# Optimization experiments

Measured on AMD Instinct MI355X. Metric: run time of the kernel, lower is better.

## Reference

```python
import jax, jax.numpy as jnp
import numpy as np

DILATIONS = [1, 2, 4, 8, 12, 24]
NUM_ITER = 10
W1 = 0.3
EPS = 1e-8
# 8-neighborhood offsets of the one-hot 3x3 kernel (center excluded)
OFFSETS = [(0, 0), (0, 1), (0, 2), (1, 0), (1, 2), (2, 0), (2, 1), (2, 2)]


def resize_bilinear_ac(x, oh, ow):
    """Bilinear resize with align_corners=True on the last two dims."""
    H, W = x.shape[-2], x.shape[-1]
    ys = jnp.linspace(0.0, H - 1.0, oh)
    xs = jnp.linspace(0.0, W - 1.0, ow)
    y0 = jnp.floor(ys).astype(jnp.int32)
    y1 = jnp.minimum(y0 + 1, H - 1)
    wy = (ys - y0).astype(x.dtype)
    x0 = jnp.floor(xs).astype(jnp.int32)
    x1 = jnp.minimum(x0 + 1, W - 1)
    wx = (xs - x0).astype(x.dtype)
    r = x[..., y0, :] * (1.0 - wy)[:, None] + x[..., y1, :] * wy[:, None]
    return r[..., x0] * (1.0 - wx) + r[..., x1] * wx


def dilated_neighbors(x, dilations):
    """Replicate-pad + gather 8 dilated neighbors per dilation.
    x: [b,c,h,w] -> [b,c,8*len(dilations),h,w] (matches one-hot conv2d emulation)."""
    b, c, h, w = x.shape
    outs = []
    for d in dilations:
        xp = jnp.pad(x, ((0, 0), (0, 0), (d, d), (d, d)), mode='edge')
        for ki, kj in OFFSETS:
            outs.append(xp[:, :, d * ki:d * ki + h, d * kj:d * kj + w])
    return jnp.stack(outs, axis=2)


def make_pos(dilations):
    base = jnp.ones(8, dtype=jnp.float32)
    base = base.at[jnp.array([0, 2, 5, 7])].set(np.sqrt(2.0).astype(np.float32))
    return jnp.concatenate([base * d for d in dilations])  # [8*D]


def setup_inputs() -> dict:
    key = jax.random.key(0)
    k1, k2 = jax.random.split(key)
    imgs = jax.random.normal(k1, (1, 3, 224, 224), dtype=jnp.float32)
    masks = jax.random.uniform(k2, (1, 21, 56, 56), dtype=jnp.float32)
    return {"imgs": imgs, "masks": masks}


def reference(imgs, masks):
    b, c, h, w = imgs.shape
    # upsample masks to image resolution
    masks = resize_bilinear_ac(masks, h, w)
    # low-res branch (scale_factor=0.3, floor like torch)
    h2, w2 = int(h * 0.3), int(w * 0.3)
    imgs2 = resize_bilinear_ac(imgs, h2, w2)

    n2 = dilated_neighbors(imgs2, DILATIONS)                     # [1,3,K,h2,w2]
    abs2 = jnp.abs(n2 - imgs2[:, :, None])
    std2 = jnp.std(n2, axis=2, keepdims=True, ddof=1)
    aff2 = (-(abs2 / (std2 + EPS)) ** 2).mean(axis=1, keepdims=True)  # [1,1,K,h2,w2]

    n1 = dilated_neighbors(imgs, DILATIONS)                      # [1,3,K,h,w]
    abs1 = jnp.abs(n1 - imgs[:, :, None])
    std1 = jnp.std(n1, axis=2, keepdims=True, ddof=1)
    aff = (-(abs1 / (std1 + EPS) / W1) ** 2).mean(axis=1, keepdims=True)  # [1,1,K,h,w]

    pos = make_pos(DILATIONS)                                    # [K]
    pos_std = jnp.std(pos, ddof=1)
    pos_aff = -((pos / (pos_std + EPS) / W1) ** 2)               # [K]

    # squeeze(0) -> bilinear upsample -> unsqueeze(0)
    aff2_up = resize_bilinear_ac(aff2[0], h, w)[None]            # [1,1,K,h,w]

    aff_total = (jax.nn.softmax(aff, axis=2)
                 + jax.nn.softmax(aff2_up, axis=2)
                 + jax.nn.softmax(pos_aff)[None, None, :, None, None])

    for _ in range(NUM_ITER):
        nm = dilated_neighbors(masks, DILATIONS)                 # [1,21,K,h,w]
        masks = (nm * aff_total).sum(axis=2)
    return masks
```

## Files before the change

kernel.cpp:

```cpp
#include <hip/hip_runtime.h>
#include <hip/hip_fp16.h>
#include <math.h>

namespace {
constexpr int IH = 224, IW = 224;
constexpr int H2 = 67, W2 = 67;
constexpr int MH = 56, MW = 56;
constexpr int CI = 3, CM = 21;
constexpr int ND = 6;
constexpr int K = 48;
constexpr int HW = IH * IW;
constexpr int HW2 = H2 * W2;
constexpr float EPS = 1e-8f;
__device__ __constant__ int DILS_C[ND] = {1, 2, 4, 8, 12, 24};
}

struct PosArr { float v[K]; };

__device__ __forceinline__ float wsum64(float v) {
    #pragma unroll
    for (int off = 1; off < 64; off <<= 1) v += __shfl_xor(v, off);
    return v;
}

__device__ __forceinline__ void gload_lds16(const void* g, void* l) {
    __builtin_amdgcn_global_load_lds(
        (const __attribute__((address_space(1))) void*)(g),
        (__attribute__((address_space(3))) void*)(l), 16, 0, 0);
}

__global__ void k_prep(const float* __restrict__ img, float* __restrict__ img2,
                       const float* __restrict__ m, __half* __restrict__ mu) {
    int t = blockIdx.x * blockDim.x + threadIdx.x;
    if (t < CI * HW2) {
        int c = t / HW2, r = t % HW2;
        int y = r / W2, x = r % W2;
        float fy = (float)y * ((float)(IH - 1) / (float)(H2 - 1));
        float fx = (float)x * ((float)(IW - 1) / (float)(W2 - 1));
        int y0 = (int)floorf(fy); int y1 = min(y0 + 1, IH - 1); float wy = fy - (float)y0;
        int x0 = (int)floorf(fx); int x1 = min(x0 + 1, IW - 1); float wx = fx - (float)x0;
        const float* p = img + c * HW;
        float v00 = p[y0 * IW + x0], v01 = p[y0 * IW + x1];
        float v10 = p[y1 * IW + x0], v11 = p[y1 * IW + x1];
        float r0 = v00 * (1.f - wy) + v10 * wy;
        float r1 = v01 * (1.f - wy) + v11 * wy;
        img2[t] = r0 * (1.f - wx) + r1 * wx;
    }
    if (t < CM * HW) {
        int c = t / HW, r = t % HW;
        int y = r / IW, x = r % IW;
        float fy = (float)y * ((float)(MH - 1) / (float)(IH - 1));
        float fx = (float)x * ((float)(MW - 1) / (float)(IW - 1));
        int y0 = (int)floorf(fy); int y1 = min(y0 + 1, MH - 1); float wy = fy - (float)y0;
        int x0 = (int)floorf(fx); int x1 = min(x0 + 1, MW - 1); float wx = fx - (float)x0;
        const float* p = m + c * MH * MW;
        float v00 = p[y0 * MW + x0], v01 = p[y0 * MW + x1];
        float v10 = p[y1 * MW + x0], v11 = p[y1 * MW + x1];
        float r0 = v00 * (1.f - wy) + v10 * wy;
        float r1 = v01 * (1.f - wy) + v11 * wy;
        mu[t] = __float2half(r0 * (1.f - wx) + r1 * wx);
    }
}

__global__ void k_aff2(const float* __restrict__ img2, float* __restrict__ aff2) {
    int gtid = blockIdx.x * blockDim.x + threadIdx.x;
    int wave = gtid >> 6;
    int lane = threadIdx.x & 63;
    if (wave >= HW2) return;
    int t = wave;
    int y = t / W2, x = t % W2;

    int k = (lane < K) ? lane : (K - 1);
    int di = k >> 3, o = k & 7;
    int d = DILS_C[di];
    int ym = max(y - d, 0), yp = min(y + d, H2 - 1);
    int xm = max(x - d, 0), xp = min(x + d, W2 - 1);
    int ki = (0x22211000u >> (o * 4)) & 3;
    int kj = (0x21020210u >> (o * 4)) & 3;
    int ry = ki == 0 ? ym : (ki == 1 ? y : yp);
    int rx = kj == 0 ? xm : (kj == 1 ? x : xp);
    int nidx = ry * W2 + rx;

    float av = 0.f;
    #pragma unroll
    for (int c = 0; c < CI; ++c) {
        const float* p = img2 + c * HW2;
        float center = p[y * W2 + x];
        float v = p[nidx];
        float vv = (lane < K) ? v : 0.f;
        float s = wsum64(vv);
        float s2 = wsum64(vv * vv);
        float mean = s * (1.f / (float)K);
        float ss = s2 - (float)K * mean * mean;
        float stdv = sqrtf(fmaxf(ss, 0.f) * (1.f / (float)(K - 1)));
        float inv = 1.f / (stdv + EPS);
        float tt = fabsf(v - center) * inv;
        av += tt * tt;
    }
    if (lane < K) aff2[(size_t)t * K + k] = av;
}

__global__ void k_aff_total(const float* __restrict__ img,
                            const float* __restrict__ aff2,
                            __half* __restrict__ afft, PosArr pos) {
    int gid = blockIdx.x * blockDim.x + threadIdx.x;
    int t = gid >> 4;
    int lane = threadIdx.x & 15;
    if (t >= HW) return;
    int y = t / IW, x = t % IW;

    int nidx[3];
    int kk[3];
    #pragma unroll
    for (int s = 0; s < 3; ++s) {
        int k = lane + 16 * s;
        kk[s] = k;
        int di = k >> 3, o = k & 7;
        int d = DILS_C[di];
        int ki = (0x22211000u >> (o * 4)) & 3;
        int kj = (0x21020210u >> (o * 4)) & 3;
        int ym = max(y - d, 0), yp = min(y + d, IH - 1);
        int xm = max(x - d, 0), xp = min(x + d, IW - 1);
        int ry = ki == 0 ? ym : (ki == 1 ? y : yp);
        int rx = kj == 0 ? xm : (kj == 1 ? x : xp);
        nidx[s] = ry * IW + rx;
    }

    float av0 = 0.f, av1 = 0.f, av2 = 0.f;
    #pragma unroll
    for (int c = 0; c < CI; ++c) {
        const float* p = img + c * HW;
        float center = p[y * IW + x];
        float n0 = p[nidx[0]], n1 = p[nidx[1]], n2 = p[nidx[2]];
        float s1 = n0 + n1 + n2;
        float s2 = n0 * n0 + n1 * n1 + n2 * n2;
        #pragma unroll
        for (int off = 1; off < 16; off <<= 1) {
            s1 += __shfl_xor(s1, off, 16);
            s2 += __shfl_xor(s2, off, 16);
        }
        float mean = s1 * (1.f / (float)K);
        float ss = s2 - (float)K * mean * mean;
        float inv = 1.f / (sqrtf(fmaxf(ss, 0.f) * (1.f / (float)(K - 1))) + EPS);
        float t0 = fabsf(n0 - center) * inv; av0 += t0 * t0;
        float t1 = fabsf(n1 - center) * inv; av1 += t1 * t1;
        float t2 = fabsf(n2 - center) * inv; av2 += t2 * t2;
    }
    const float sc = -(1.f / (float)CI) / (0.3f * 0.3f);
    av0 *= sc; av1 *= sc; av2 *= sc;
    float m1 = fmaxf(av0, fmaxf(av1, av2));
    #pragma unroll
    for (int off = 1; off < 16; off <<= 1) m1 = fmaxf(m1, __shfl_xor(m1, off, 16));
    float e0 = expf(av0 - m1), e1 = expf(av1 - m1), e2 = expf(av2 - m1);
    float es = e0 + e1 + e2;
    #pragma unroll
    for (int off = 1; off < 16; off <<= 1) es += __shfl_xor(es, off, 16);
    float r1 = 1.f / es;

    float fy = (float)y * ((float)(H2 - 1) / (float)(IH - 1));
    float fx = (float)x * ((float)(W2 - 1) / (float)(IW - 1));
    int y0 = (int)floorf(fy); int y1 = min(y0 + 1, H2 - 1); float wy = fy - (float)y0;
    int x0 = (int)floorf(fx); int x1 = min(x0 + 1, W2 - 1); float wx = fx - (float)x0;
    const float* q00 = aff2 + (size_t)(y0 * W2 + x0) * K;
    const float* q01 = aff2 + (size_t)(y0 * W2 + x1) * K;
    const float* q10 = aff2 + (size_t)(y1 * W2 + x0) * K;
    const float* q11 = aff2 + (size_t)(y1 * W2 + x1) * K;
    float w00 = (1.f - wy) * (1.f - wx), w01 = (1.f - wy) * wx;
    float w10 = wy * (1.f - wx), w11 = wy * wx;
    const float sc2 = -(1.f / (float)CI);
    float b0 = (q00[kk[0]] * w00 + q01[kk[0]] * w01 + q10[kk[0]] * w10 + q11[kk[0]] * w11) * sc2;
    float b1 = (q00[kk[1]] * w00 + q01[kk[1]] * w01 + q10[kk[1]] * w10 + q11[kk[1]] * w11) * sc2;
    float b2 = (q00[kk[2]] * w00 + q01[kk[2]] * w01 + q10[kk[2]] * w10 + q11[kk[2]] * w11) * sc2;
    float m2 = fmaxf(b0, fmaxf(b1, b2));
    #pragma unroll
    for (int off = 1; off < 16; off <<= 1) m2 = fmaxf(m2, __shfl_xor(m2, off, 16));
    float f0 = expf(b0 - m2), f1 = expf(b1 - m2), f2 = expf(b2 - m2);
    float fs = f0 + f1 + f2;
    #pragma unroll
    for (int off = 1; off < 16; off <<= 1) fs += __shfl_xor(fs, off, 16);
    float r2 = 1.f / fs;

    __half* o = afft + (size_t)t * K;
    o[kk[0]] = __float2half(e0 * r1 + f0 * r2 + pos.v[kk[0]]);
    o[kk[1]] = __float2half(e1 * r1 + f1 * r2 + pos.v[kk[1]]);
    o[kk[2]] = __float2half(e2 * r1 + f2 * r2 + pos.v[kk[2]]);
}

template<bool LAST>
__global__ __launch_bounds__(256) void k_prop(const __half* __restrict__ min_,
                                              const __half* __restrict__ afft,
                                              void* __restrict__ mout) {
    __shared__ __half L[13 * 224];
    int tid = threadIdx.x;
    int bid = blockIdx.x;
    int sw = (bid & 7) * 588 + (bid >> 3);
    int y = sw / 21;
    int c = sw - y * 21;

    int x = min(tid, IW - 1);
    int t = y * IW + x;
    uint4 w[6];
    {
        const uint4* aw = (const uint4*)(afft + (size_t)t * K);
        #pragma unroll
        for (int i = 0; i < 6; ++i) w[i] = aw[i];
    }

    const int ROW_DY[13] = {-24, -12, -8, -4, -2, -1, 0, 1, 2, 4, 8, 12, 24};
    const __half* mc = min_ + (size_t)c * HW;
    {
        int i = tid;
        int r = i / 28, q = i - r * 28;
        int gy = min(max(y + ROW_DY[r], 0), IH - 1);
        gload_lds16(mc + gy * IW + q * 8, L + i * 8);
    }
    if (tid < 108) {
        int i = tid + 256;
        int r = i / 28, q = i - r * 28;
        int gy = min(max(y + ROW_DY[r], 0), IH - 1);
        gload_lds16(mc + gy * IW + q * 8, L + i * 8);
    }
    __syncthreads();

    if (tid >= IW) return;

    const int DILS[ND] = {1, 2, 4, 8, 12, 24};
    const int RMI[ND] = {5, 4, 3, 2, 1, 0};
    const int RPI[ND] = {7, 8, 9, 10, 11, 12};
    const __half* Lc = L + 6 * 224;

    float acc = 0.f;
    #pragma unroll
    for (int di = 0; di < ND; ++di) {
        int d = DILS[di];
        int cm = max(x - d, 0);
        int cp = min(x + d, IW - 1);
        const __half* Lm = L + RMI[di] * 224;
        const __half* Lp = L + RPI[di] * 224;
        const __half2* hp = (const __half2*)&w[di];
        float2 f01 = __half22float2(hp[0]);
        float2 f23 = __half22float2(hp[1]);
        float2 f45 = __half22float2(hp[2]);
        float2 f67 = __half22float2(hp[3]);
        acc += __half2float(Lm[cm]) * f01.x;
        acc += __half2float(Lm[x])  * f01.y;
        acc += __half2float(Lm[cp]) * f23.x;
        acc += __half2float(Lc[cm]) * f23.y;
        acc += __half2float(Lc[cp]) * f45.x;
        acc += __half2float(Lp[cm]) * f45.y;
        acc += __half2float(Lp[x])  * f67.x;
        acc += __half2float(Lp[cp]) * f67.y;
    }
    if (LAST) {
        ((float*)mout)[(size_t)c * HW + t] = acc;
    } else {
        ((__half*)mout)[(size_t)c * HW + t] = __float2half(acc);
    }
}

extern "C" void kernel_launch(void* const* d_in, const int* in_sizes, int n_in,
                              void* d_out, int out_size, void* d_ws, size_t ws_size,
                              hipStream_t stream) {
    const float* imgs  = (const float*)d_in[0];
    const float* masks = (const float*)d_in[1];
    float* out = (float*)d_out;

    float* ws = (float*)d_ws;
    float* imgs2 = ws;
    float* aff2  = imgs2 + 16384;
    __half* afft = (__half*)(aff2 + K * HW2);
    __half* mA   = afft + (size_t)K * HW;
    __half* mB   = mA + (size_t)CM * HW;

    PosArr pos;
    {
        double pv[K];
        const int dil[ND] = {1, 2, 4, 8, 12, 24};
        const double s2 = sqrt(2.0);
        for (int di = 0; di < ND; ++di)
            for (int o = 0; o < 8; ++o) {
                double base = (o == 0 || o == 2 || o == 5 || o == 7) ? s2 : 1.0;
                pv[di * 8 + o] = base * (double)dil[di];
            }
        double sum = 0.0; for (int k = 0; k < K; ++k) sum += pv[k];
        double mean = sum / K;
        double ssd = 0.0; for (int k = 0; k < K; ++k) { double d0 = pv[k] - mean; ssd += d0 * d0; }
        double stdv = sqrt(ssd / (K - 1));
        double pa[K];
        double mx = -1e300;
        for (int k = 0; k < K; ++k) {
            double u = pv[k] / (stdv + 1e-8) / 0.3;
            pa[k] = -u * u;
            if (pa[k] > mx) mx = pa[k];
        }
        double es = 0.0, ev[K];
        for (int k = 0; k < K; ++k) { ev[k] = exp(pa[k] - mx); es += ev[k]; }
        for (int k = 0; k < K; ++k) pos.v[k] = (float)(ev[k] / es);
    }

    dim3 blk(256);
    k_prep<<<(CM * HW + 255) / 256, blk, 0, stream>>>(imgs, imgs2, masks, mA);
    k_aff2<<<(HW2 * 64 + 255) / 256, blk, 0, stream>>>(imgs2, aff2);
    k_aff_total<<<(HW * 16 + 255) / 256, blk, 0, stream>>>(imgs, aff2, afft, pos);

    __half* bufs[2] = {mA, mB};
    const __half* cur = mA;
    for (int i = 0; i < 9; ++i) {
        __half* o = bufs[(i + 1) & 1];
        k_prop<false><<<4704, blk, 0, stream>>>(cur, afft, (void*)o);
        cur = o;
    }
    k_prop<true><<<4704, blk, 0, stream>>>(cur, afft, (void*)out);
}
```

Baseline: 170.3 us.

## Process three row-channel tiles per block with double-buffered LDS prefetch

Each k_prop block now handles three (row, channel) work items instead of one, and launches a third as many blocks. While one tile is being computed, the 13-row mask stencil for the next tile is loaded asynchronously into a second LDS buffer, so load latency overlaps with compute. The cost is doubled shared memory, extra barriers, and fewer blocks in flight, which may reduce occupancy and the latency hiding that came from many independent blocks.

Result: slower. 183.2 us (+7.5%).

```diff
diff --git a/kernel.cpp b/kernel.cpp
--- a/kernel.cpp
+++ b/kernel.cpp
@@ -190,71 +190,95 @@
 __global__ __launch_bounds__(256) void k_prop(const __half* __restrict__ min_,
                                               const __half* __restrict__ afft,
                                               void* __restrict__ mout) {
-    __shared__ __half L[13 * 224];
-    int tid = threadIdx.x;
-    int bid = blockIdx.x;
-    int sw = (bid & 7) * 588 + (bid >> 3);
-    int y = sw / 21;
-    int c = sw - y * 21;
-
-    int x = min(tid, IW - 1);
-    int t = y * IW + x;
-    uint4 w[6];
+    __shared__ __half L[2][13 * 224];
+    const int tid = threadIdx.x;
+    const int bid = blockIdx.x;
+    const int base = (bid & 7) * 588 + (bid >> 3);
+    const int ROW_DY[13] = {-24, -12, -8, -4, -2, -1, 0, 1, 2, 4, 8, 12, 24};
+    const int x = min(tid, IW - 1);
+
+    int yy[3], cc[3];
+    #pragma unroll
+    for (int j = 0; j < 3; ++j) {
+        int sw = base + j * 196;
+        yy[j] = sw / 21;
+        cc[j] = sw - yy[j] * 21;
+    }
+
     {
-        const uint4* aw = (const uint4*)(afft + (size_t)t * K);
-        #pragma unroll
-        for (int i = 0; i < 6; ++i) w[i] = aw[i];
-    }
-
-    const int ROW_DY[13] = {-24, -12, -8, -4, -2, -1, 0, 1, 2, 4, 8, 12, 24};
-    const __half* mc = min_ + (size_t)c * HW;
-    {
-        int i = tid;
-        int r = i / 28, q = i - r * 28;
-        int gy = min(max(y + ROW_DY[r], 0), IH - 1);
-        gload_lds16(mc + gy * IW + q * 8, L + i * 8);
-    }
-    if (tid < 108) {
-        int i = tid + 256;
-        int r = i / 28, q = i - r * 28;
-        int gy = min(max(y + ROW_DY[r], 0), IH - 1);
-        gload_lds16(mc + gy * IW + q * 8, L + i * 8);
+        const __half* mc = min_ + (size_t)cc[0] * HW;
+        int i = tid, r = i / 28, q = i - r * 28;
+        int gy = min(max(yy[0] + ROW_DY[r], 0), IH - 1);
+        gload_lds16(mc + gy * IW + q * 8, &L[0][i * 8]);
+        if (tid < 108) {
+            int i2 = tid + 256, r2 = i2 / 28, q2 = i2 - r2 * 28;
+            int gy2 = min(max(yy[0] + ROW_DY[r2], 0), IH - 1);
+            gload_lds16(mc + gy2 * IW + q2 * 8, &L[0][i2 * 8]);
+        }
     }
     __syncthreads();
 
-    if (tid >= IW) return;
-
-    const int DILS[ND] = {1, 2, 4, 8, 12, 24};
-    const int RMI[ND] = {5, 4, 3, 2, 1, 0};
-    const int RPI[ND] = {7, 8, 9, 10, 11, 12};
-    const __half* Lc = L + 6 * 224;
-
-    float acc = 0.f;
-    #pragma unroll
-    for (int di = 0; di < ND; ++di) {
-        int d = DILS[di];
-        int cm = max(x - d, 0);
-        int cp = min(x + d, IW - 1);
-        const __half* Lm = L + RMI[di] * 224;
-        const __half* Lp = L + RPI[di] * 224;
-        const __half2* hp = (const __half2*)&w[di];
-        float2 f01 = __half22float2(hp[0]);
-        float2 f23 = __half22float2(hp[1]);
-        float2 f45 = __half22float2(hp[2]);
-        float2 f67 = __half22float2(hp[3]);
-        acc += __half2float(Lm[cm]) * f01.x;
-        acc += __half2float(Lm[x])  * f01.y;
-        acc += __half2float(Lm[cp]) * f23.x;
-        acc += __half2float(Lc[cm]) * f23.y;
-        acc += __half2float(Lc[cp]) * f45.x;
-        acc += __half2float(Lp[cm]) * f45.y;
-        acc += __half2float(Lp[x])  * f67.x;
-        acc += __half2float(Lp[cp]) * f67.y;
-    }
-    if (LAST) {
-        ((float*)mout)[(size_t)c * HW + t] = acc;
-    } else {
-        ((__half*)mout)[(size_t)c * HW + t] = __float2half(acc);
+    #pragma unroll
+    for (int j = 0; j < 3; ++j) {
+        const __half* Lb = L[j & 1];
+        const int y = yy[j], c = cc[j];
+        const int t = y * IW + x;
+
+        uint4 w[6];
+        {
+            const uint4* aw = (const uint4*)(afft + (size_t)t * K);
+            #pragma unroll
+            for (int i = 0; i < 6; ++i) w[i] = aw[i];
+        }
+
+        if (j < 2) {
+            __half* Ln = L[(j + 1) & 1];
+            const __half* mc = min_ + (size_t)cc[j + 1] * HW;
+            int i = tid, r = i / 28, q = i - r * 28;
+            int gy = min(max(yy[j + 1] + ROW_DY[r], 0), IH - 1);
+            gload_lds16(mc + gy * IW + q * 8, Ln + i * 8);
+            if (tid < 108) {
+                int i2 = tid + 256, r2 = i2 / 28, q2 = i2 - r2 * 28;
+                int gy2 = min(max(yy[j + 1] + ROW_DY[r2], 0), IH - 1);
+                gload_lds16(mc + gy2 * IW + q2 * 8, Ln + i2 * 8);
+            }
+        }
+
+        if (tid < IW) {
+            const int DILS[ND] = {1, 2, 4, 8, 12, 24};
+            const int RMI[ND] = {5, 4, 3, 2, 1, 0};
+            const int RPI[ND] = {7, 8, 9, 10, 11, 12};
+            const __half* Lc = Lb + 6 * 224;
+            float acc = 0.f;
+            #pragma unroll
+            for (int di = 0; di < ND; ++di) {
+                int d = DILS[di];
+                int cm = max(x - d, 0);
+                int cp = min(x + d, IW - 1);
+                const __half* Lm = Lb + RMI[di] * 224;
+                const __half* Lp = Lb + RPI[di] * 224;
+                const __half2* hp = (const __half2*)&w[di];
+                float2 f01 = __half22float2(hp[0]);
+                float2 f23 = __half22float2(hp[1]);
+                float2 f45 = __half22float2(hp[2]);
+                float2 f67 = __half22float2(hp[3]);
+                acc += __half2float(Lm[cm]) * f01.x;
+                acc += __half2float(Lm[x])  * f01.y;
+                acc += __half2float(Lm[cp]) * f23.x;
+                acc += __half2float(Lc[cm]) * f23.y;
+                acc += __half2float(Lc[cp]) * f45.x;
+                acc += __half2float(Lp[cm]) * f45.y;
+                acc += __half2float(Lp[x])  * f67.x;
+                acc += __half2float(Lp[cp]) * f67.y;
+            }
+            if (LAST) {
+                ((float*)mout)[(size_t)c * HW + t] = acc;
+            } else {
+                ((__half*)mout)[(size_t)c * HW + t] = __float2half(acc);
+            }
+        }
+
+        if (j < 2) __syncthreads();
     }
 }
 
@@ -307,8 +331,8 @@
     const __half* cur = mA;
     for (int i = 0; i < 9; ++i) {
         __half* o = bufs[(i + 1) & 1];
-        k_prop<false><<<4704, blk, 0, stream>>>(cur, afft, (void*)o);
+        k_prop<false><<<1568, blk, 0, stream>>>(cur, afft, (void*)o);
         cur = o;
     }
-    k_prop<true><<<4704, blk, 0, stream>>>(cur, afft, (void*)out);
-}
+    k_prop<true><<<1568, blk, 0, stream>>>(cur, afft, (void*)out);
+}
```

## Pad LDS rows with replicated edges and compute two pixels per thread

Applied to the files above, without the earlier changes.

The propagation kernel now stores each mask row in shared memory with 24-element replicated halos on both sides. This removes the per-neighbor clamping and lets even/odd pixel pairs read neighbors as aligned half2 loads. Each of 112 threads now computes two adjacent output pixels and writes them as a packed pair. The cost is an extra barrier and halo-fill step, larger LDS rows, and fewer active threads per block.

New measurement: 222.0 us. +30.3%, slower.

```diff
diff --git a/kernel.cpp b/kernel.cpp
--- a/kernel.cpp
+++ b/kernel.cpp
@@ -12,6 +12,7 @@
 constexpr int HW = IH * IW;
 constexpr int HW2 = H2 * W2;
 constexpr float EPS = 1e-8f;
+constexpr int RS = 272;
 __device__ __constant__ int DILS_C[ND] = {1, 2, 4, 8, 12, 24};
 }
 
@@ -190,71 +191,118 @@
 __global__ __launch_bounds__(256) void k_prop(const __half* __restrict__ min_,
                                               const __half* __restrict__ afft,
                                               void* __restrict__ mout) {
-    __shared__ __half L[13 * 224];
-    int tid = threadIdx.x;
-    int bid = blockIdx.x;
-    int sw = (bid & 7) * 588 + (bid >> 3);
-    int y = sw / 21;
-    int c = sw - y * 21;
-
-    int x = min(tid, IW - 1);
-    int t = y * IW + x;
-    uint4 w[6];
-    {
-        const uint4* aw = (const uint4*)(afft + (size_t)t * K);
-        #pragma unroll
-        for (int i = 0; i < 6; ++i) w[i] = aw[i];
-    }
-
+    __shared__ __half L[13 * RS];
+    const int tid = threadIdx.x;
+    const int bid = blockIdx.x;
+    const int sw = (bid & 7) * 588 + (bid >> 3);
+    const int y = sw / 21;
+    const int c = sw - y * 21;
     const int ROW_DY[13] = {-24, -12, -8, -4, -2, -1, 0, 1, 2, 4, 8, 12, 24};
     const __half* mc = min_ + (size_t)c * HW;
+
+    const int j0 = 2 * min(tid, 111);
+    const int t0 = y * IW + j0;
+    uint4 w0[6], w1[6];
+    if (tid < 112) {
+        const uint4* aw0 = (const uint4*)(afft + (size_t)t0 * K);
+        const uint4* aw1 = (const uint4*)(afft + (size_t)(t0 + 1) * K);
+        #pragma unroll
+        for (int i = 0; i < 6; ++i) { w0[i] = aw0[i]; w1[i] = aw1[i]; }
+    }
+
+    __half hv;
+    int fr = 0, fh = 0;
+    if (tid < 78) {
+        fr = tid / 6; fh = tid - fr * 6;
+        int gy = min(max(y + ROW_DY[fr], 0), IH - 1);
+        hv = mc[gy * IW + ((fh < 3) ? 0 : (IW - 1))];
+    }
+
     {
         int i = tid;
-        int r = i / 28, q = i - r * 28;
+        int r = i / 34, s = i - r * 34;
         int gy = min(max(y + ROW_DY[r], 0), IH - 1);
-        gload_lds16(mc + gy * IW + q * 8, L + i * 8);
-    }
-    if (tid < 108) {
+        int off = min(max((s - 3) * 8, 0), 216);
+        gload_lds16(mc + gy * IW + off, L + i * 8);
+    }
+    if (tid < 186) {
         int i = tid + 256;
-        int r = i / 28, q = i - r * 28;
+        int r = i / 34, s = i - r * 34;
         int gy = min(max(y + ROW_DY[r], 0), IH - 1);
-        gload_lds16(mc + gy * IW + q * 8, L + i * 8);
-    }
+        int off = min(max((s - 3) * 8, 0), 216);
+        gload_lds16(mc + gy * IW + off, L + i * 8);
+    }
+
     __syncthreads();
-
-    if (tid >= IW) return;
-
-    const int DILS[ND] = {1, 2, 4, 8, 12, 24};
+    if (tid < 78) {
+        unsigned short us = __half_as_ushort(hv);
+        unsigned int dd = (unsigned int)us | ((unsigned int)us << 16);
+        uint4 splat = make_uint4(dd, dd, dd, dd);
+        int off = fr * RS + ((fh < 3) ? fh * 8 : 248 + (fh - 3) * 8);
+        *(uint4*)(L + off) = splat;
+    }
+    __syncthreads();
+
+    if (tid >= 112) return;
+
     const int RMI[ND] = {5, 4, 3, 2, 1, 0};
     const int RPI[ND] = {7, 8, 9, 10, 11, 12};
-    const __half* Lc = L + 6 * 224;
-
-    float acc = 0.f;
-    #pragma unroll
-    for (int di = 0; di < ND; ++di) {
-        int d = DILS[di];
-        int cm = max(x - d, 0);
-        int cp = min(x + d, IW - 1);
-        const __half* Lm = L + RMI[di] * 224;
-        const __half* Lp = L + RPI[di] * 224;
-        const __half2* hp = (const __half2*)&w[di];
-        float2 f01 = __half22float2(hp[0]);
-        float2 f23 = __half22float2(hp[1]);
-        float2 f45 = __half22float2(hp[2]);
-        float2 f67 = __half22float2(hp[3]);
-        acc += __half2float(Lm[cm]) * f01.x;
-        acc += __half2float(Lm[x])  * f01.y;
-        acc += __half2float(Lm[cp]) * f23.x;
-        acc += __half2float(Lc[cm]) * f23.y;
-        acc += __half2float(Lc[cp]) * f45.x;
-        acc += __half2float(Lp[cm]) * f45.y;
-        acc += __half2float(Lp[x])  * f67.x;
-        acc += __half2float(Lp[cp]) * f67.y;
-    }
+    const __half* B = L + 24 + j0;
+    const __half* Lc = B + 6 * RS;
+    float acc0 = 0.f, acc1 = 0.f;
+
+    {
+        const __half* Lm = B + RMI[0] * RS;
+        const __half* Lp = B + RPI[0] * RS;
+        const __half2* h0 = (const __half2*)&w0[0];
+        const __half2* h1 = (const __half2*)&w1[0];
+        float2 a01 = __half22float2(h0[0]), a23 = __half22float2(h0[1]);
+        float2 a45 = __half22float2(h0[2]), a67 = __half22float2(h0[3]);
+        float2 b01 = __half22float2(h1[0]), b23 = __half22float2(h1[1]);
+        float2 b45 = __half22float2(h1[2]), b67 = __half22float2(h1[3]);
+        float m_1 = __half2float(Lm[-1]), m0 = __half2float(Lm[0]);
+        float m1v = __half2float(Lm[1]),  m2 = __half2float(Lm[2]);
+        float c_1 = __half2float(Lc[-1]), c0 = __half2float(Lc[0]);
+        float c1v = __half2float(Lc[1]),  c2 = __half2float(Lc[2]);
+        float p_1 = __half2float(Lp[-1]), p0 = __half2float(Lp[0]);
+        float p1v = __half2float(Lp[1]),  p2 = __half2float(Lp[2]);
+        acc0 += m_1 * a01.x + m0 * a01.y + m1v * a23.x + c_1 * a23.y
+              + c1v * a45.x + p_1 * a45.y + p0 * a67.x + p1v * a67.y;
+        acc1 += m0 * b01.x + m1v * b01.y + m2 * b23.x + c0 * b23.y
+              + c2 * b45.x + p0 * b45.y + p1v * b67.x + p2 * b67.y;
+    }
+
+    const int DILS[ND] = {1, 2, 4, 8, 12, 24};
+    #pragma unroll
+    for (int di = 1; di < ND; ++di) {
+        const int d = DILS[di];
+        const __half* Lm = B + RMI[di] * RS;
+        const __half* Lp = B + RPI[di] * RS;
+        const __half2* h0 = (const __half2*)&w0[di];
+        const __half2* h1 = (const __half2*)&w1[di];
+        float2 a01 = __half22float2(h0[0]), a23 = __half22float2(h0[1]);
+        float2 a45 = __half22float2(h0[2]), a67 = __half22float2(h0[3]);
+        float2 b01 = __half22float2(h1[0]), b23 = __half22float2(h1[1]);
+        float2 b45 = __half22float2(h1[2]), b67 = __half22float2(h1[3]);
+        float2 vmm = __half22float2(*(const __half2*)(Lm - d));
+        float2 vm0 = __half22float2(*(const __half2*)(Lm));
+        float2 vmp = __half22float2(*(const __half2*)(Lm + d));
+        float2 vcm = __half22float2(*(const __half2*)(Lc - d));
+        float2 vcp = __half22float2(*(const __half2*)(Lc + d));
+        float2 vpm = __half22float2(*(const __half2*)(Lp - d));
+        float2 vp0 = __half22float2(*(const __half2*)(Lp));
+        float2 vpp = __half22float2(*(const __half2*)(Lp + d));
+        acc0 += vmm.x * a01.x + vm0.x * a01.y + vmp.x * a23.x + vcm.x * a23.y
+              + vcp.x * a45.x + vpm.x * a45.y + vp0.x * a67.x + vpp.x * a67.y;
+        acc1 += vmm.y * b01.x + vm0.y * b01.y + vmp.y * b23.x + vcm.y * b23.y
+              + vcp.y * b45.x + vpm.y * b45.y + vp0.y * b67.x + vpp.y * b67.y;
+    }
+
     if (LAST) {
-        ((float*)mout)[(size_t)c * HW + t] = acc;
+        *(float2*)((float*)mout + (size_t)c * HW + t0) = make_float2(acc0, acc1);
     } else {
-        ((__half*)mout)[(size_t)c * HW + t] = __float2half(acc);
+        *(__half2*)((__half*)mout + (size_t)c * HW + t0) =
+            __floats2half2_rn(acc0, acc1);
     }
 }
 
```
